# Performance work log

Measured on AMD Instinct MI355X. Metric: run time of the kernel, lower is better.

The kernel has to match this reference:

```python
import jax, jax.numpy as jnp
import numpy as np

B, C, H, W = 8, 128, 64, 64   # batch, hidden_dim, spatial
CIN = 192                      # input_dim
N, K, R, DFF = 1, 4, 8, 512    # d_state, scan dirs, dt_rank=ceil(128/16), mlp hidden
EPS = 1e-5


def _conv1x1(t, w, b=None):
    y = jnp.einsum('bchw,oc->bohw', t, w)
    return y + b[None, :, None, None] if b is not None else y


def _ln_cf(t, g, bta):
    # LayerNorm over channel dim (channel_first)
    mu = t.mean(1, keepdims=True)
    var = ((t - mu) ** 2).mean(1, keepdims=True)
    return (t - mu) * jax.lax.rsqrt(var + EPS) * g[None, :, None, None] + bta[None, :, None, None]


def _forward(h, cz, cr, cq, x,
             in_proj_w, in_proj_b, ln1_g, ln1_b,
             ssm_in_w, conv_w, conv_b,
             x_proj_w, dt_w, dt_b, A_logs, Ds,
             outnorm_g, outnorm_b, out_proj_w,
             ln2_g, ln2_b, fc1_w, fc1_b, fc2_w, fc2_b,
             gate_w, gate_b):
    combined = jnp.concatenate([h, x], axis=1)          # [B, C+CIN, H, W]
    feat = _conv1x1(combined, in_proj_w, in_proj_b)     # [B, C, H, W]

    # ---- SS2D (v2_noz, channel_first) ----
    u = _conv1x1(_ln_cf(feat, ln1_g, ln1_b), ssm_in_w)  # in_proj (no bias)
    u = jax.lax.conv_general_dilated(u, conv_w, (1, 1), [(1, 1), (1, 1)],
                                     dimension_numbers=('NCHW', 'OIHW', 'NCHW'),
                                     feature_group_count=C)
    u = jax.nn.silu(u + conv_b[None, :, None, None])

    L = H * W
    x0 = u.reshape(B, C, L)
    x1 = u.transpose(0, 1, 3, 2).reshape(B, C, L)       # column-major scan
    xs = jnp.stack([x0, x1, x0[..., ::-1], x1[..., ::-1]], axis=1)  # [B,K,C,L]

    x_dbl = jnp.einsum('bkcl,kdc->bkdl', xs, x_proj_w)  # [B,K,R+2N,L]
    dts, Bs, Cs = jnp.split(x_dbl, [R, R + N], axis=2)
    delta = jax.nn.softplus(jnp.einsum('bkrl,kcr->bkcl', dts, dt_w) + dt_b[None, :, :, None])
    A = -jnp.exp(A_logs).reshape(K, C, N)
    D = Ds.reshape(K, C)

    dA = jnp.exp(delta[..., None] * A[None, :, :, None, :])                   # [B,K,C,L,N]
    dBu = (delta * xs)[..., None] * Bs.transpose(0, 1, 3, 2)[:, :, None, :, :]  # [B,K,C,L,N]

    def step(hst, inp):
        dA_t, dBu_t, C_t = inp
        hst = dA_t * hst + dBu_t                         # [B,K,C,N]
        return hst, jnp.einsum('bkcn,bkn->bkc', hst, C_t)

    init = jnp.zeros((B, K, C, N), u.dtype)
    _, ys = jax.lax.scan(step, init,
                         (dA.transpose(3, 0, 1, 2, 4),
                          dBu.transpose(3, 0, 1, 2, 4),
                          Cs.transpose(3, 0, 1, 2)))
    ys = ys.transpose(1, 2, 3, 0)                        # [B,K,C,L]
    ys = ys + D[None, :, :, None] * xs

    # cross-merge: undo flips and transposes, sum directions
    y = ys[:, 0] + ys[:, 2, :, ::-1]
    y_t = ys[:, 1] + ys[:, 3, :, ::-1]
    y = y + y_t.reshape(B, C, W, H).transpose(0, 1, 3, 2).reshape(B, C, L)
    y = y.reshape(B, C, H, W)
    y = _ln_cf(y, outnorm_g, outnorm_b)
    ssm_out = _conv1x1(y, out_proj_w)

    # ---- VSSBlock residuals (drop_path identity in eval) ----
    z = feat + ssm_out
    m = _conv1x1(_ln_cf(z, ln2_g, ln2_b), fc1_w, fc1_b)
    m = jax.nn.gelu(m, approximate=False)
    m = _conv1x1(m, fc2_w, fc2_b)
    z = z + m

    # ---- gated update ----
    g = jax.nn.sigmoid(_conv1x1(z, gate_w, gate_b))
    return g * z + (1.0 - g) * h


def setup_inputs() -> dict:
    key = jax.random.key(0)
    ks = jax.random.split(key, 20)
    rn = lambda i, shape, s=0.02: jax.random.normal(ks[i], shape, jnp.float32) * s
    return dict(
        h=jax.random.normal(ks[0], (B, C, H, W), jnp.float32),
        cz=jax.random.normal(ks[1], (B, C, H, W), jnp.float32),
        cr=jax.random.normal(ks[2], (B, C, H, W), jnp.float32),
        cq=jax.random.normal(ks[3], (B, C, H, W), jnp.float32),
        x=jax.random.normal(ks[4], (B, CIN, H, W), jnp.float32),
        in_proj_w=rn(5, (C, C + CIN)), in_proj_b=jnp.zeros(C, jnp.float32),
        ln1_g=jnp.ones(C, jnp.float32), ln1_b=jnp.zeros(C, jnp.float32),
        ssm_in_w=rn(6, (C, C)),
        conv_w=rn(7, (C, 1, 3, 3), 0.1), conv_b=jnp.zeros(C, jnp.float32),
        x_proj_w=rn(8, (K, R + 2 * N, C)),
        dt_w=rn(9, (K, C, R), 0.1), dt_b=rn(10, (K, C), 0.1),
        A_logs=jnp.zeros((K * C, N), jnp.float32),
        Ds=jnp.ones(K * C, jnp.float32),
        outnorm_g=jnp.ones(C, jnp.float32), outnorm_b=jnp.zeros(C, jnp.float32),
        out_proj_w=rn(11, (C, C)),
        ln2_g=jnp.ones(C, jnp.float32), ln2_b=jnp.zeros(C, jnp.float32),
        fc1_w=rn(12, (DFF, C)), fc1_b=jnp.zeros(DFF, jnp.float32),
        fc2_w=rn(13, (C, DFF)), fc2_b=jnp.zeros(C, jnp.float32),
        gate_w=rn(14, (C, C)), gate_b=jnp.zeros(C, jnp.float32),
    )


def reference(h, cz, cr, cq, x,
              in_proj_w, in_proj_b, ln1_g, ln1_b,
              ssm_in_w, conv_w, conv_b,
              x_proj_w, dt_w, dt_b, A_logs, Ds,
              outnorm_g, outnorm_b, out_proj_w,
              ln2_g, ln2_b, fc1_w, fc1_b, fc2_w, fc2_b,
              gate_w, gate_b):
    return _forward(h, cz, cr, cq, x,
                    in_proj_w, in_proj_b, ln1_g, ln1_b,
                    ssm_in_w, conv_w, conv_b,
                    x_proj_w, dt_w, dt_b, A_logs, Ds,
                    outnorm_g, outnorm_b, out_proj_w,
                    ln2_g, ln2_b, fc1_w, fc1_b, fc2_w, fc2_b,
                    gate_w, gate_b)
```

## Files before the change

kernel.cpp:

```cpp
#include <hip/hip_runtime.h>
#include <hip/hip_bf16.h>

constexpr int B_ = 8, C_ = 128, Hh = 64, Ww = 64, L_ = Hh * Ww;
constexpr int CIN_ = 192, K_ = 4, Rr = 8, DFF_ = 512;
constexpr long SZ1 = (long)B_ * C_ * L_;
constexpr float EPSf = 1e-5f;
constexpr float LOG2E = 1.44269504088896f;
constexpr float LN2f  = 0.693147180559945f;

#define DEVI __device__ __forceinline__

using s16x4 = __attribute__((ext_vector_type(4))) short;
using s16x8 = __attribute__((ext_vector_type(8))) short;
using f32x4 = __attribute__((ext_vector_type(4))) float;

DEVI float sigm(float x) { return 1.f / (1.f + __expf(-x)); }
DEVI float geluf(float x) { return 0.5f * x * (1.f + erff(x * 0.70710678118654752f)); }
DEVI float siluf(float x) { return x * sigm(x); }

DEVI unsigned short f2bf(float f) {
    unsigned u = __float_as_uint(f);
    u += 0x7fffu + ((u >> 16) & 1u);
    return (unsigned short)(u >> 16);
}

DEVI int tadr(int pos) { return ((pos & 63) << 6) | (pos >> 6); }

template <int BN, bool ACC, bool BIAS, bool XGELU, bool SIG, bool GATE, bool SPLIT>
__global__ __launch_bounds__(256) void gemm_k(
    const float* __restrict__ W, const float* __restrict__ X1, long sX1,
    const float* __restrict__ X2, long sX2, int splitRow,
    const float* __restrict__ bias, float* __restrict__ Cp, long sC,
    int M, int N, int K)
{
    constexpr int NI = BN / 32;
    __shared__ unsigned short sA[128][40];
    __shared__ unsigned short sB[BN][40];
    const int tid = threadIdx.x;
    const int bn = blockIdx.x, bm = blockIdx.y, bz = blockIdx.z;
    const float* X1b = X1 + (long)bz * sX1;
    const float* X2b = (SPLIT || GATE) ? (X2 + (long)bz * sX2) : nullptr;
    float* Cb = Cp + (long)bz * sC;
    const int n0 = bn * BN, m0 = bm * 128;

    const int l = tid & 63, w = tid >> 6;
    const int wm = w >> 1, wn = w & 1;
    const int lr = l & 15, lk = (l >> 4) * 8;

    const int awrow = tid >> 1, awk = (tid & 1) * 16;

    f32x4 acc[4][NI];
#pragma unroll
    for (int i = 0; i < 4; i++)
#pragma unroll
        for (int j = 0; j < NI; j++) acc[i][j] = (f32x4)0.f;

    for (int k0 = 0; k0 < K; k0 += 32) {
        {
            const float* wp = W + (long)(m0 + awrow) * K + k0 + awk;
            float4 f0 = *(const float4*)(wp + 0);
            float4 f1 = *(const float4*)(wp + 4);
            float4 f2 = *(const float4*)(wp + 8);
            float4 f3 = *(const float4*)(wp + 12);
            s16x8 v0, v1;
            v0[0]=f2bf(f0.x); v0[1]=f2bf(f0.y); v0[2]=f2bf(f0.z); v0[3]=f2bf(f0.w);
            v0[4]=f2bf(f1.x); v0[5]=f2bf(f1.y); v0[6]=f2bf(f1.z); v0[7]=f2bf(f1.w);
            v1[0]=f2bf(f2.x); v1[1]=f2bf(f2.y); v1[2]=f2bf(f2.z); v1[3]=f2bf(f2.w);
            v1[4]=f2bf(f3.x); v1[5]=f2bf(f3.y); v1[6]=f2bf(f3.z); v1[7]=f2bf(f3.w);
            *(s16x8*)&sA[awrow][awk] = v0;
            *(s16x8*)&sA[awrow][awk + 8] = v1;
        }
        if constexpr (BN == 128) {
            const int bnb = tid & 31, bkb = tid >> 5;
            const int krow = k0 + bkb * 4;
            const float* xp;
            if (SPLIT && krow >= splitRow)
                xp = X2b + (long)(krow - splitRow) * N + n0 + bnb * 4;
            else
                xp = X1b + (long)krow * N + n0 + bnb * 4;
            float4 r0 = *(const float4*)(xp + 0 * (long)N);
            float4 r1 = *(const float4*)(xp + 1 * (long)N);
            float4 r2 = *(const float4*)(xp + 2 * (long)N);
            float4 r3 = *(const float4*)(xp + 3 * (long)N);
            if (XGELU) {
                r0.x=geluf(r0.x); r0.y=geluf(r0.y); r0.z=geluf(r0.z); r0.w=geluf(r0.w);
                r1.x=geluf(r1.x); r1.y=geluf(r1.y); r1.z=geluf(r1.z); r1.w=geluf(r1.w);
                r2.x=geluf(r2.x); r2.y=geluf(r2.y); r2.z=geluf(r2.z); r2.w=geluf(r2.w);
                r3.x=geluf(r3.x); r3.y=geluf(r3.y); r3.z=geluf(r3.z); r3.w=geluf(r3.w);
            }
            const float* p0 = (const float*)&r0;
            const float* p1 = (const float*)&r1;
            const float* p2 = (const float*)&r2;
            const float* p3 = (const float*)&r3;
#pragma unroll
            for (int c = 0; c < 4; c++) {
                s16x4 v;
                v[0] = f2bf(p0[c]); v[1] = f2bf(p1[c]);
                v[2] = f2bf(p2[c]); v[3] = f2bf(p3[c]);
                *(s16x4*)&sB[bnb * 4 + c][bkb * 4] = v;
            }
        } else {
            const int bnb = tid & 15, bkb = tid >> 4;
            const int krow = k0 + bkb * 2;
            const int col0 = n0 + bnb * 4;
            const float* xpa;
            const float* xpb;
            if (SPLIT && krow >= splitRow)
                xpa = X2b + (long)(krow - splitRow) * N + col0;
            else
                xpa = X1b + (long)krow * N + col0;
            if (SPLIT && (krow + 1) >= splitRow)
                xpb = X2b + (long)(krow + 1 - splitRow) * N + col0;
            else
                xpb = X1b + (long)(krow + 1) * N + col0;
            float4 r0 = *(const float4*)xpa;
            float4 r1 = *(const float4*)xpb;
            if (XGELU) {
                r0.x=geluf(r0.x); r0.y=geluf(r0.y); r0.z=geluf(r0.z); r0.w=geluf(r0.w);
                r1.x=geluf(r1.x); r1.y=geluf(r1.y); r1.z=geluf(r1.z); r1.w=geluf(r1.w);
            }
            const float* p0 = (const float*)&r0;
            const float* p1 = (const float*)&r1;
#pragma unroll
            for (int c = 0; c < 4; c++) {
                unsigned v = (unsigned)f2bf(p0[c]) | ((unsigned)f2bf(p1[c]) << 16);
                *(unsigned*)&sB[bnb * 4 + c][bkb * 2] = v;
            }
        }
        __syncthreads();
        s16x8 af[4], bf[NI];
#pragma unroll
        for (int mi = 0; mi < 4; mi++) af[mi] = *(const s16x8*)&sA[wm * 64 + mi * 16 + lr][lk];
#pragma unroll
        for (int ni = 0; ni < NI; ni++) bf[ni] = *(const s16x8*)&sB[wn * (BN / 2) + ni * 16 + lr][lk];
#pragma unroll
        for (int mi = 0; mi < 4; mi++)
#pragma unroll
            for (int ni = 0; ni < NI; ni++)
                acc[mi][ni] = __builtin_amdgcn_mfma_f32_16x16x32_bf16(af[mi], bf[ni], acc[mi][ni], 0, 0, 0);
        __syncthreads();
    }

#pragma unroll
    for (int mi = 0; mi < 4; mi++) {
#pragma unroll
        for (int r = 0; r < 4; r++) {
            const int row = m0 + wm * 64 + mi * 16 + (l >> 4) * 4 + r;
            const float bv = BIAS ? bias[row] : 0.f;
#pragma unroll
            for (int ni = 0; ni < NI; ni++) {
                const int col = n0 + wn * (BN / 2) + ni * 16 + lr;
                float* cp = Cb + (long)row * N + col;
                float v = acc[mi][ni][r] + bv;
                if (ACC) v += *cp;
                if (SIG) v = sigm(v);
                if (GATE) {
                    v = sigm(v);
                    float zv = X1b[(long)row * N + col];
                    float hv = X2b[(long)row * N + col];
                    v = hv + v * (zv - hv);
                }
                *cp = v;
            }
        }
    }
}

__global__ __launch_bounds__(256) void ln_cf_k(const float* __restrict__ in,
                                               const float* __restrict__ g,
                                               const float* __restrict__ bta,
                                               float* __restrict__ out)
{
    __shared__ float s1[4][64], s2[4][64];
    const int tid = threadIdx.x;
    const int p = tid & 63, q = tid >> 6;
    const long posg = (long)blockIdx.x * 64 + p;
    const int b = (int)(posg / L_);
    const int pp = (int)(posg % L_);
    const float* base = in + ((long)b * C_ + q * 32) * L_ + pp;
    float v[32];
    float s = 0.f, sq = 0.f;
#pragma unroll
    for (int i = 0; i < 32; i++) {
        float t = base[(long)i * L_];
        v[i] = t; s += t; sq += t * t;
    }
    s1[q][p] = s; s2[q][p] = sq;
    __syncthreads();
    float ts = s1[0][p] + s1[1][p] + s1[2][p] + s1[3][p];
    float tq = s2[0][p] + s2[1][p] + s2[2][p] + s2[3][p];
    float mu = ts * (1.f / 128.f);
    float var = tq * (1.f / 128.f) - mu * mu;
    float rs = rsqrtf(var + EPSf);
    float* ob = out + ((long)b * C_ + q * 32) * L_ + pp;
#pragma unroll
    for (int i = 0; i < 32; i++) {
        int c = q * 32 + i;
        ob[(long)i * L_] = (v[i] - mu) * rs * g[c] + bta[c];
    }
}

__global__ __launch_bounds__(256) void dwconvT_k(const float* __restrict__ in,
                                                 const float* __restrict__ wts,
                                                 const float* __restrict__ bias,
                                                 float* __restrict__ uo,
                                                 float* __restrict__ uTo)
{
    __shared__ float t[64][65];
    const long plane = blockIdx.x;
    const int c = (int)(plane & 127);
    const int tid = threadIdx.x;
    const float* src = in + plane * (long)L_;
#pragma unroll
    for (int ii = 0; ii < 16; ii++) {
        int idx = tid + ii * 256;
        t[idx >> 6][idx & 63] = src[idx];
    }
    float kw[9];
#pragma unroll
    for (int q = 0; q < 9; q++) kw[q] = wts[c * 9 + q];
    const float bc = bias[c];
    __syncthreads();
    float r[16];
#pragma unroll
    for (int ii = 0; ii < 16; ii++) {
        int idx = tid + ii * 256;
        int h = idx >> 6, w2 = idx & 63;
        float acc = bc;
#pragma unroll
        for (int dh = -1; dh <= 1; dh++) {
            int hh = h + dh;
            if ((unsigned)hh >= 64u) continue;
#pragma unroll
            for (int dw = -1; dw <= 1; dw++) {
                int ww2 = w2 + dw;
                if ((unsigned)ww2 >= 64u) continue;
                acc += t[hh][ww2] * kw[(dh + 1) * 3 + (dw + 1)];
            }
        }
        r[ii] = siluf(acc);
    }
    __syncthreads();
    float* ud = uo + plane * (long)L_;
#pragma unroll
    for (int ii = 0; ii < 16; ii++) {
        int idx = tid + ii * 256;
        t[idx >> 6][idx & 63] = r[ii];
        ud[idx] = r[ii];
    }
    __syncthreads();
    float* utd = uTo + plane * (long)L_;
#pragma unroll
    for (int ii = 0; ii < 16; ii++) {
        int idx = tid + ii * 256;
        utd[idx] = t[idx & 63][idx >> 6];
    }
}

template <bool ADD>
__global__ __launch_bounds__(256) void transp_k(const float* __restrict__ src,
                                                float* __restrict__ dst)
{
    __shared__ float t[64][65];
    const long plane = blockIdx.x;
    const float* s = src + plane * (long)L_;
    float* d = dst + plane * (long)L_;
    const int tid = threadIdx.x;
#pragma unroll
    for (int i = 0; i < 16; i++) {
        int idx = tid + i * 256;
        t[idx >> 6][idx & 63] = s[idx];
    }
    __syncthreads();
#pragma unroll
    for (int i = 0; i < 16; i++) {
        int idx = tid + i * 256;
        int r = idx >> 6, cc = idx & 63;
        float val = t[cc][r];
        if (ADD) d[idx] += val; else d[idx] = val;
    }
}

__global__ __launch_bounds__(256) void xdbl2_k(const float* __restrict__ u,
                                               const float* __restrict__ uT,
                                               const float* __restrict__ xw,
                                               float* __restrict__ out)
{
    __shared__ float wsm[2][16][132];
    const int pair = blockIdx.y, b = blockIdx.z;
    const int tid = threadIdx.x;
#pragma unroll
    for (int i = 0; i < 8; i++) {
        int idx = tid * 8 + i;
        wsm[0][idx >> 7][idx & 127] = xw[pair * 2048 + idx];
        wsm[1][idx >> 7][idx & 127] = xw[(pair + 2) * 2048 + idx];
    }
    __syncthreads();
    const int dg = (tid & 3) * 4;
    const int lo = tid >> 2;
    const int pos = blockIdx.x * 64 + lo;
    const float* usrc = (pair ? uT : u) + (long)b * C_ * L_ + pos;
    float a0[4] = {0.f, 0.f, 0.f, 0.f};
    float a1[4] = {0.f, 0.f, 0.f, 0.f};
#pragma unroll 4
    for (int c = 0; c < C_; c++) {
        float uc = usrc[(long)c * L_];
#pragma unroll
        for (int j = 0; j < 4; j++) {
            a0[j] += wsm[0][dg + j][c] * uc;
            a1[j] += wsm[1][dg + j][c] * uc;
        }
    }
    const long baseA = ((long)(b * K_ + pair) * L_) << 4;
    const long baseB = ((long)(b * K_ + pair + 2) * L_) << 4;
    const int s  = tadr(pos);
    const int s2 = tadr(L_ - 1 - pos);
    *(float4*)(out + baseA + ((long)s  << 4) + dg) = make_float4(a0[0], a0[1], a0[2], a0[3]);
    *(float4*)(out + baseB + ((long)s2 << 4) + dg) = make_float4(a1[0], a1[1], a1[2], a1[3]);
}

__global__ __launch_bounds__(256) void scan_ph1L_k(const float* __restrict__ xdbl,
                                                   const float* __restrict__ u,
                                                   const float* __restrict__ uT,
                                                   const float* __restrict__ dtw,
                                                   const float* __restrict__ dtb,
                                                   const float* __restrict__ alogs,
                                                   float* __restrict__ st)
{
    __shared__ float xtf[2][32][16];
    __shared__ float xtb[2][32][16];
    const int bid = blockIdx.x;
    const int jj = bid & 63, kh = (bid >> 6) & 1, b = bid >> 7;
    const int t = threadIdx.x;
    const int kf = kh, kb = kh + 2;
    const float* xf = xdbl + ((long)(b * 4 + kf) << 16);
    const float* xb = xdbl + ((long)(b * 4 + kb) << 16);
    {
        const int q = t & 3, i = (t >> 2) & 31, j2 = t >> 7;
        const int jf = 2 * jj + j2, jB = 127 - jf;
        const int sf = (((jf & 1) * 32 + i) << 6) | (jf >> 1);
        const int sb = (((jB & 1) * 32 + i) << 6) | (jB >> 1);
        *(float4*)&xtf[j2][i][q * 4] = *(const float4*)(xf + (long)sf * 16 + q * 4);
        *(float4*)&xtb[j2][i][q * 4] = *(const float4*)(xb + (long)sb * 16 + q * 4);
    }
    const int c = t & 127, jh = t >> 7;
    const int jf = 2 * jj + jh, jB = 127 - jf;
    const float* uplane = (kh ? uT : u) + (long)(b * 128 + c) * L_;
    float ur[32];
    {
        const float* up = uplane + jf * 32;
#pragma unroll
        for (int q = 0; q < 8; q++) *(float4*)&ur[q * 4] = *(const float4*)(up + q * 4);
    }
    __syncthreads();
    {
        float dw[8];
#pragma unroll
        for (int r = 0; r < 8; r++) dw[r] = dtw[((kf * 128 + c) << 3) + r];
        const float db = dtb[kf * 128 + c];
        float An[4];
#pragma unroll
        for (int n = 0; n < 4; n++) An[n] = -__expf(alogs[((kf * 128 + c) << 2) + n]);
        float P0 = 1.f, P1 = 1.f, P2 = 1.f, P3 = 1.f;
        float S0 = 0.f, S1 = 0.f, S2 = 0.f, S3 = 0.f;
#pragma unroll
        for (int i = 0; i < 32; i++) {
            const float* xr = xtf[jh][i];
            float z = db + xr[0]*dw[0] + xr[1]*dw[1] + xr[2]*dw[2] + xr[3]*dw[3]
                         + xr[4]*dw[4] + xr[5]*dw[5] + xr[6]*dw[6] + xr[7]*dw[7];
            float wv = (z > 15.f) ? z * LOG2E : log2f(1.f + __expf(z));
            float dl = wv * LN2f;
            float du = dl * ur[i];
            float e;
            e = exp2f(wv * An[0]); S0 = e * S0 + du * xr[8];  P0 *= e;
            e = exp2f(wv * An[1]); S1 = e * S1 + du * xr[9];  P1 *= e;
            e = exp2f(wv * An[2]); S2 = e * S2 + du * xr[10]; P2 *= e;
            e = exp2f(wv * An[3]); S3 = e * S3 + du * xr[11]; P3 *= e;
        }
        float* o = st + ((long)((b * 4 + kf) * 128 + c) << 10) + (jf << 3);
        *(float4*)o = make_float4(P0, P1, P2, P3);
        *(float4*)(o + 4) = make_float4(S0, S1, S2, S3);
    }
    {
        float dw[8];
#pragma unroll
        for (int r = 0; r < 8; r++) dw[r] = dtw[((kb * 128 + c) << 3) + r];
        const float db = dtb[kb * 128 + c];
        float An[4];
#pragma unroll
        for (int n = 0; n < 4; n++) An[n] = -__expf(alogs[((kb * 128 + c) << 2) + n]);
        float P0 = 1.f, P1 = 1.f, P2 = 1.f, P3 = 1.f;
        float S0 = 0.f, S1 = 0.f, S2 = 0.f, S3 = 0.f;
#pragma unroll
        for (int i = 0; i < 32; i++) {
            const float* xr = xtb[jh][i];
            float z = db + xr[0]*dw[0] + xr[1]*dw[1] + xr[2]*dw[2] + xr[3]*dw[3]
                         + xr[4]*dw[4] + xr[5]*dw[5] + xr[6]*dw[6] + xr[7]*dw[7];
            float wv = (z > 15.f) ? z * LOG2E : log2f(1.f + __expf(z));
            float dl = wv * LN2f;
            float du = dl * ur[31 - i];
            float e;
            e = exp2f(wv * An[0]); S0 = e * S0 + du * xr[8];  P0 *= e;
            e = exp2f(wv * An[1]); S1 = e * S1 + du * xr[9];  P1 *= e;
            e = exp2f(wv * An[2]); S2 = e * S2 + du * xr[10]; P2 *= e;
            e = exp2f(wv * An[3]); S3 = e * S3 + du * xr[11]; P3 *= e;
        }
        float* o = st + ((long)((b * 4 + kb) * 128 + c) << 10) + (jB << 3);
        *(float4*)o = make_float4(P0, P1, P2, P3);
        *(float4*)(o + 4) = make_float4(S0, S1, S2, S3);
    }
}

__global__ __launch_bounds__(256) void scan_mid_k(float* __restrict__ st)
{
    const long t = (long)blockIdx.x * 256 + threadIdx.x;
    const long chain = t >> 6;
    const int ln = (int)(t & 63);
    float* base = st + (chain << 10) + (ln << 4);
    float4 Pa = *(float4*)(base + 0);
    float4 Sa = *(float4*)(base + 4);
    float4 Pb = *(float4*)(base + 8);
    float4 Sb = *(float4*)(base + 12);
    float4 P, S;
    P.x = Pb.x * Pa.x; P.y = Pb.y * Pa.y; P.z = Pb.z * Pa.z; P.w = Pb.w * Pa.w;
    S.x = Sb.x + Pb.x * Sa.x; S.y = Sb.y + Pb.y * Sa.y;
    S.z = Sb.z + Pb.z * Sa.z; S.w = Sb.w + Pb.w * Sa.w;
#pragma unroll
    for (int d = 1; d < 64; d <<= 1) {
        float4 Pu, Su;
        Pu.x = __shfl_up(P.x, d, 64); Pu.y = __shfl_up(P.y, d, 64);
        Pu.z = __shfl_up(P.z, d, 64); Pu.w = __shfl_up(P.w, d, 64);
        Su.x = __shfl_up(S.x, d, 64); Su.y = __shfl_up(S.y, d, 64);
        Su.z = __shfl_up(S.z, d, 64); Su.w = __shfl_up(S.w, d, 64);
        if (ln >= d) {
            S.x += P.x * Su.x; S.y += P.y * Su.y;
            S.z += P.z * Su.z; S.w += P.w * Su.w;
            P.x *= Pu.x; P.y *= Pu.y; P.z *= Pu.z; P.w *= Pu.w;
        }
    }
    float4 E;
    E.x = __shfl_up(S.x, 1, 64); E.y = __shfl_up(S.y, 1, 64);
    E.z = __shfl_up(S.z, 1, 64); E.w = __shfl_up(S.w, 1, 64);
    if (ln == 0) { E.x = 0.f; E.y = 0.f; E.z = 0.f; E.w = 0.f; }
    float4 E1;
    E1.x = Sa.x + Pa.x * E.x; E1.y = Sa.y + Pa.y * E.y;
    E1.z = Sa.z + Pa.z * E.z; E1.w = Sa.w + Pa.w * E.w;
    *(float4*)(base + 4)  = E;
    *(float4*)(base + 12) = E1;
}

__global__ __launch_bounds__(256) void scan_ph2L_k(const float* __restrict__ xdbl,
                                                   const float* __restrict__ u,
                                                   const float* __restrict__ uT,
                                                   const float* __restrict__ dtw,
                                                   const float* __restrict__ dtb,
                                                   const float* __restrict__ alogs,
                                                   const float* __restrict__ Dsp,
                                                   const float* __restrict__ st,
                                                   float* __restrict__ Y0,
                                                   float* __restrict__ Yt)
{
    __shared__ float xtf[2][32][16];
    __shared__ float xtb[2][32][16];
    __shared__ float yt[128][65];
    const int bid = blockIdx.x;
    const int jj = bid & 63, kh = (bid >> 6) & 1, b = bid >> 7;
    const int t = threadIdx.x;
    const int kf = kh, kb = kh + 2;
    const float* xf = xdbl + ((long)(b * 4 + kf) << 16);
    const float* xb = xdbl + ((long)(b * 4 + kb) << 16);
    {
        const int q = t & 3, i = (t >> 2) & 31, j2 = t >> 7;
        const int jf = 2 * jj + j2, jB = 127 - jf;
        const int sf = (((jf & 1) * 32 + i) << 6) | (jf >> 1);
        const int sb = (((jB & 1) * 32 + i) << 6) | (jB >> 1);
        *(float4*)&xtf[j2][i][q * 4] = *(const float4*)(xf + (long)sf * 16 + q * 4);
        *(float4*)&xtb[j2][i][q * 4] = *(const float4*)(xb + (long)sb * 16 + q * 4);
    }
    const int c = t & 127, jh = t >> 7;
    const int jf = 2 * jj + jh, jB = 127 - jf;
    const float* uplane = (kh ? uT : u) + (long)(b * 128 + c) * L_;
    float ur[32];
    {
        const float* up = uplane + jf * 32;
#pragma unroll
        for (int q = 0; q < 8; q++) *(float4*)&ur[q * 4] = *(const float4*)(up + q * 4);
    }
    __syncthreads();
    {
        float dw[8];
#pragma unroll
        for (int r = 0; r < 8; r++) dw[r] = dtw[((kf * 128 + c) << 3) + r];
        const float db = dtb[kf * 128 + c];
        float An[4];
#pragma unroll
        for (int n = 0; n < 4; n++) An[n] = -__expf(alogs[((kf * 128 + c) << 2) + n]);
        const float Dc = Dsp[kf * 128 + c];
        float4 H = *(const float4*)(st + ((long)((b * 4 + kf) * 128 + c) << 10) + (jf << 3) + 4);
        float h0 = H.x, h1 = H.y, h2 = H.z, h3 = H.w;
#pragma unroll
        for (int i = 0; i < 32; i++) {
            const float* xr = xtf[jh][i];
            float z = db + xr[0]*dw[0] + xr[1]*dw[1] + xr[2]*dw[2] + xr[3]*dw[3]
                         + xr[4]*dw[4] + xr[5]*dw[5] + xr[6]*dw[6] + xr[7]*dw[7];
            float wv = (z > 15.f) ? z * LOG2E : log2f(1.f + __expf(z));
            float dl = wv * LN2f;
            float du = dl * ur[i];
            float e;
            e = exp2f(wv * An[0]); h0 = e * h0 + du * xr[8];
            e = exp2f(wv * An[1]); h1 = e * h1 + du * xr[9];
            e = exp2f(wv * An[2]); h2 = e * h2 + du * xr[10];
            e = exp2f(wv * An[3]); h3 = e * h3 + du * xr[11];
            yt[c][jh * 32 + i] = h0 * xr[12] + h1 * xr[13] + h2 * xr[14] + h3 * xr[15] + Dc * ur[i];
        }
    }
    {
        float dw[8];
#pragma unroll
        for (int r = 0; r < 8; r++) dw[r] = dtw[((kb * 128 + c) << 3) + r];
        const float db = dtb[kb * 128 + c];
        float An[4];
#pragma unroll
        for (int n = 0; n < 4; n++) An[n] = -__expf(alogs[((kb * 128 + c) << 2) + n]);
        const float Dc = Dsp[kb * 128 + c];
        float4 H = *(const float4*)(st + ((long)((b * 4 + kb) * 128 + c) << 10) + (jB << 3) + 4);
        float h0 = H.x, h1 = H.y, h2 = H.z, h3 = H.w;
#pragma unroll
        for (int i = 0; i < 32; i++) {
            const float* xr = xtb[jh][i];
            float z = db + xr[0]*dw[0] + xr[1]*dw[1] + xr[2]*dw[2] + xr[3]*dw[3]
                         + xr[4]*dw[4] + xr[5]*dw[5] + xr[6]*dw[6] + xr[7]*dw[7];
            float wv = (z > 15.f) ? z * LOG2E : log2f(1.f + __expf(z));
            float dl = wv * LN2f;
            float uv = ur[31 - i];
            float du = dl * uv;
            float e;
            e = exp2f(wv * An[0]); h0 = e * h0 + du * xr[8];
            e = exp2f(wv * An[1]); h1 = e * h1 + du * xr[9];
            e = exp2f(wv * An[2]); h2 = e * h2 + du * xr[10];
            e = exp2f(wv * An[3]); h3 = e * h3 + du * xr[11];
            yt[c][jh * 32 + 31 - i] += h0 * xr[12] + h1 * xr[13] + h2 * xr[14] + h3 * xr[15] + Dc * uv;
        }
    }
    __syncthreads();
    float* ydst = (kh ? Yt : Y0) + (long)(b * 128) * L_ + jj * 64;
    const int pos = t & 63, cg = t >> 6;
#pragma unroll
    for (int rep = 0; rep < 32; rep++) {
        const int c2 = cg + rep * 4;
        ydst[(long)c2 * L_ + pos] = yt[c2][pos];
    }
}

extern "C" void kernel_launch(void* const* d_in, const int* in_sizes, int n_in,
                              void* d_out, int out_size, void* d_ws, size_t ws_size,
                              hipStream_t stream)
{
    const float* h_in      = (const float*)d_in[0];
    const float* x_in      = (const float*)d_in[4];
    const float* in_proj_w = (const float*)d_in[5];
    const float* in_proj_b = (const float*)d_in[6];
    const float* ln1_g     = (const float*)d_in[7];
    const float* ln1_b     = (const float*)d_in[8];
    const float* ssm_in_w  = (const float*)d_in[9];
    const float* conv_w    = (const float*)d_in[10];
    const float* conv_b    = (const float*)d_in[11];
    const float* x_proj_w  = (const float*)d_in[12];
    const float* dt_w      = (const float*)d_in[13];
    const float* dt_b      = (const float*)d_in[14];
    const float* A_logs    = (const float*)d_in[15];
    const float* Dsp       = (const float*)d_in[16];
    const float* outnorm_g = (const float*)d_in[17];
    const float* outnorm_b = (const float*)d_in[18];
    const float* out_proj_w= (const float*)d_in[19];
    const float* ln2_g     = (const float*)d_in[20];
    const float* ln2_b     = (const float*)d_in[21];
    const float* fc1_w     = (const float*)d_in[22];
    const float* fc1_b     = (const float*)d_in[23];
    const float* fc2_w     = (const float*)d_in[24];
    const float* fc2_b     = (const float*)d_in[25];
    const float* gate_w    = (const float*)d_in[26];
    const float* gate_b    = (const float*)d_in[27];

    float* ws   = (float*)d_ws;
    float* fz   = ws;
    float* ubuf = ws + SZ1;
    float* tbuf = ws + 2 * SZ1;
    float* ybuf = ws + 3 * SZ1;
    float* xdbl = ws + 4 * SZ1;
    float* stbf = ws + 4 * SZ1 + 2097152;
    float* mbuf = ubuf;
    float* gbuf = (float*)d_out;

    const dim3 blk(256);
    const long sBC = (long)C_ * L_;
    const long sX  = (long)CIN_ * L_;
    const long sM  = (long)DFF_ * L_;

    gemm_k<64, false, true, false, false, false, true><<<dim3(64, 1, 8), blk, 0, stream>>>(
        in_proj_w, h_in, sBC, x_in, sX, 128, in_proj_b, fz, sBC, 128, L_, 320);
    ln_cf_k<<<dim3(512), blk, 0, stream>>>(fz, ln1_g, ln1_b, ybuf);
    gemm_k<64, false, false, false, false, false, false><<<dim3(64, 1, 8), blk, 0, stream>>>(
        ssm_in_w, ybuf, sBC, nullptr, 0, 1 << 30, nullptr, tbuf, sBC, 128, L_, 128);
    dwconvT_k<<<dim3(1024), blk, 0, stream>>>(tbuf, conv_w, conv_b, ubuf, ybuf);
    xdbl2_k<<<dim3(64, 2, 8), blk, 0, stream>>>(ubuf, ybuf, x_proj_w, xdbl);
    scan_ph1L_k<<<dim3(1024), blk, 0, stream>>>(xdbl, ubuf, ybuf, dt_w, dt_b, A_logs, stbf);
    scan_mid_k<<<dim3(1024), blk, 0, stream>>>(stbf);
    scan_ph2L_k<<<dim3(1024), blk, 0, stream>>>(xdbl, ubuf, ybuf, dt_w, dt_b,
                                                A_logs, Dsp, stbf, tbuf, gbuf);
    transp_k<true><<<dim3(1024), blk, 0, stream>>>(gbuf, tbuf);
    ln_cf_k<<<dim3(512), blk, 0, stream>>>(tbuf, outnorm_g, outnorm_b, ybuf);
    gemm_k<64, true, false, false, false, false, false><<<dim3(64, 1, 8), blk, 0, stream>>>(
        out_proj_w, ybuf, sBC, nullptr, 0, 1 << 30, nullptr, fz, sBC, 128, L_, 128);
    ln_cf_k<<<dim3(512), blk, 0, stream>>>(fz, ln2_g, ln2_b, gbuf);
    gemm_k<128, false, true, false, false, false, false><<<dim3(32, 4, 8), blk, 0, stream>>>(
        fc1_w, gbuf, sBC, nullptr, 0, 1 << 30, fc1_b, mbuf, sM, 512, L_, 128);
    gemm_k<64, true, true, true, false, false, false><<<dim3(64, 1, 8), blk, 0, stream>>>(
        fc2_w, mbuf, sM, nullptr, 0, 1 << 30, fc2_b, fz, sBC, 128, L_, 512);
    gemm_k<64, false, true, false, false, true, false><<<dim3(64, 1, 8), blk, 0, stream>>>(
        gate_w, fz, sBC, h_in, sBC, 1 << 30, gate_b, (float*)d_out, sBC, 128, L_, 128);
}
```

Baseline: 256.0 us.

## Fuse channel LayerNorms into GEMM prologue/epilogue and vectorize scan LDS reads

The first LayerNorm is folded into the in_proj GEMM epilogue, which reduces per-column statistics across the full 128-row M tile and writes the normalized output directly. For outnorm, a small stats-only kernel computes mean and rstd, and the out_proj GEMM applies the normalization while loading its B operand. That same GEMM then also emits the ln2 output in its epilogue. This removes three full read+write passes of the activation tensor and two kernel launches, at the cost of extra registers and shared memory in the GEMM. The scan loops also replace scalar shared-memory reads with float4 loads.

```diff
diff --git a/kernel.cpp b/kernel.cpp
--- a/kernel.cpp
+++ b/kernel.cpp
@@ -26,12 +26,16 @@
 
 DEVI int tadr(int pos) { return ((pos & 63) << 6) | (pos >> 6); }
 
-template <int BN, bool ACC, bool BIAS, bool XGELU, bool SIG, bool GATE, bool SPLIT>
+template <int BN, bool ACC, bool BIAS, bool XGELU, bool SIG, bool GATE, bool SPLIT,
+          bool XLN, bool LNOUT>
 __global__ __launch_bounds__(256) void gemm_k(
     const float* __restrict__ W, const float* __restrict__ X1, long sX1,
     const float* __restrict__ X2, long sX2, int splitRow,
-    const float* __restrict__ bias, float* __restrict__ Cp, long sC,
-    int M, int N, int K)
+    const float* __restrict__ bias,
+    const float* __restrict__ xmu, const float* __restrict__ xrs,
+    const float* __restrict__ xg, const float* __restrict__ xbt,
+    float* __restrict__ NOut, const float* __restrict__ og, const float* __restrict__ obt,
+    float* __restrict__ Cp, long sC, int M, int N, int K)
 {
     constexpr int NI = BN / 32;
     __shared__ unsigned short sA[128][40];
@@ -115,6 +119,16 @@
                 xpb = X1b + (long)(krow + 1) * N + col0;
             float4 r0 = *(const float4*)xpa;
             float4 r1 = *(const float4*)xpb;
+            if (XLN) {
+                float4 m4 = *(const float4*)(xmu + (long)bz * N + col0);
+                float4 s4 = *(const float4*)(xrs + (long)bz * N + col0);
+                float ga = xg[krow], be = xbt[krow];
+                r0.x=(r0.x-m4.x)*s4.x*ga+be; r0.y=(r0.y-m4.y)*s4.y*ga+be;
+                r0.z=(r0.z-m4.z)*s4.z*ga+be; r0.w=(r0.w-m4.w)*s4.w*ga+be;
+                ga = xg[krow + 1]; be = xbt[krow + 1];
+                r1.x=(r1.x-m4.x)*s4.x*ga+be; r1.y=(r1.y-m4.y)*s4.y*ga+be;
+                r1.z=(r1.z-m4.z)*s4.z*ga+be; r1.w=(r1.w-m4.w)*s4.w*ga+be;
+            }
             if (XGELU) {
                 r0.x=geluf(r0.x); r0.y=geluf(r0.y); r0.z=geluf(r0.z); r0.w=geluf(r0.w);
                 r1.x=geluf(r1.x); r1.y=geluf(r1.y); r1.z=geluf(r1.z); r1.w=geluf(r1.w);
@@ -141,6 +155,11 @@
         __syncthreads();
     }
 
+    float ps[NI], pq[NI];
+    if (LNOUT) {
+#pragma unroll
+        for (int ni = 0; ni < NI; ni++) { ps[ni] = 0.f; pq[ni] = 0.f; }
+    }
 #pragma unroll
     for (int mi = 0; mi < 4; mi++) {
 #pragma unroll
@@ -161,15 +180,66 @@
                     v = hv + v * (zv - hv);
                 }
                 *cp = v;
-            }
-        }
-    }
-}
-
-__global__ __launch_bounds__(256) void ln_cf_k(const float* __restrict__ in,
-                                               const float* __restrict__ g,
-                                               const float* __restrict__ bta,
-                                               float* __restrict__ out)
+                if (LNOUT) {
+                    acc[mi][ni][r] = v;
+                    ps[ni] += v; pq[ni] += v * v;
+                }
+            }
+        }
+    }
+    if constexpr (LNOUT) {
+        __shared__ float redS[2][2][NI][16];
+        __shared__ float redQ[2][2][NI][16];
+        __shared__ float muL[BN], rsL[BN];
+#pragma unroll
+        for (int ni = 0; ni < NI; ni++) {
+            ps[ni] += __shfl_xor(ps[ni], 16, 64);
+            ps[ni] += __shfl_xor(ps[ni], 32, 64);
+            pq[ni] += __shfl_xor(pq[ni], 16, 64);
+            pq[ni] += __shfl_xor(pq[ni], 32, 64);
+        }
+        if (l < 16) {
+#pragma unroll
+            for (int ni = 0; ni < NI; ni++) {
+                redS[wm][wn][ni][l] = ps[ni];
+                redQ[wm][wn][ni][l] = pq[ni];
+            }
+        }
+        __syncthreads();
+        if (tid < BN) {
+            const int cc = tid;
+            const int wn2 = cc >> 5, rem = cc & 31;
+            const int ni2 = rem >> 4, lr2 = rem & 15;
+            float s = redS[0][wn2][ni2][lr2] + redS[1][wn2][ni2][lr2];
+            float q = redQ[0][wn2][ni2][lr2] + redQ[1][wn2][ni2][lr2];
+            float mu = s * (1.f / 128.f);
+            float var = q * (1.f / 128.f) - mu * mu;
+            muL[cc] = mu;
+            rsL[cc] = rsqrtf(var + EPSf);
+        }
+        __syncthreads();
+        float* Nb = NOut + (long)bz * sC;
+#pragma unroll
+        for (int mi = 0; mi < 4; mi++) {
+#pragma unroll
+            for (int r = 0; r < 4; r++) {
+                const int row = m0 + wm * 64 + mi * 16 + (l >> 4) * 4 + r;
+                const float gg = og[row], bb = obt[row];
+#pragma unroll
+                for (int ni = 0; ni < NI; ni++) {
+                    const int cc = wn * (BN / 2) + ni * 16 + lr;
+                    const int col = n0 + cc;
+                    float v = acc[mi][ni][r];
+                    Nb[(long)row * N + col] = (v - muL[cc]) * rsL[cc] * gg + bb;
+                }
+            }
+        }
+    }
+}
+
+__global__ __launch_bounds__(256) void ln_stats_k(const float* __restrict__ in,
+                                                  float* __restrict__ mu,
+                                                  float* __restrict__ rs)
 {
     __shared__ float s1[4][64], s2[4][64];
     const int tid = threadIdx.x;
@@ -178,25 +248,21 @@
     const int b = (int)(posg / L_);
     const int pp = (int)(posg % L_);
     const float* base = in + ((long)b * C_ + q * 32) * L_ + pp;
-    float v[32];
     float s = 0.f, sq = 0.f;
 #pragma unroll
     for (int i = 0; i < 32; i++) {
         float t = base[(long)i * L_];
-        v[i] = t; s += t; sq += t * t;
+        s += t; sq += t * t;
     }
     s1[q][p] = s; s2[q][p] = sq;
     __syncthreads();
-    float ts = s1[0][p] + s1[1][p] + s1[2][p] + s1[3][p];
-    float tq = s2[0][p] + s2[1][p] + s2[2][p] + s2[3][p];
-    float mu = ts * (1.f / 128.f);
-    float var = tq * (1.f / 128.f) - mu * mu;
-    float rs = rsqrtf(var + EPSf);
-    float* ob = out + ((long)b * C_ + q * 32) * L_ + pp;
-#pragma unroll
-    for (int i = 0; i < 32; i++) {
-        int c = q * 32 + i;
-        ob[(long)i * L_] = (v[i] - mu) * rs * g[c] + bta[c];
+    if (q == 0) {
+        float ts = s1[0][p] + s1[1][p] + s1[2][p] + s1[3][p];
+        float tq = s2[0][p] + s2[1][p] + s2[2][p] + s2[3][p];
+        float m = ts * (1.f / 128.f);
+        float var = tq * (1.f / 128.f) - m * m;
+        mu[posg] = m;
+        rs[posg] = rsqrtf(var + EPSf);
     }
 }
 
@@ -365,17 +431,19 @@
         float S0 = 0.f, S1 = 0.f, S2 = 0.f, S3 = 0.f;
 #pragma unroll
         for (int i = 0; i < 32; i++) {
-            const float* xr = xtf[jh][i];
-            float z = db + xr[0]*dw[0] + xr[1]*dw[1] + xr[2]*dw[2] + xr[3]*dw[3]
-                         + xr[4]*dw[4] + xr[5]*dw[5] + xr[6]*dw[6] + xr[7]*dw[7];
+            float4 x0 = *(const float4*)&xtf[jh][i][0];
+            float4 x1 = *(const float4*)&xtf[jh][i][4];
+            float4 xs = *(const float4*)&xtf[jh][i][8];
+            float z = db + x0.x*dw[0] + x0.y*dw[1] + x0.z*dw[2] + x0.w*dw[3]
+                         + x1.x*dw[4] + x1.y*dw[5] + x1.z*dw[6] + x1.w*dw[7];
             float wv = (z > 15.f) ? z * LOG2E : log2f(1.f + __expf(z));
             float dl = wv * LN2f;
             float du = dl * ur[i];
             float e;
-            e = exp2f(wv * An[0]); S0 = e * S0 + du * xr[8];  P0 *= e;
-            e = exp2f(wv * An[1]); S1 = e * S1 + du * xr[9];  P1 *= e;
-            e = exp2f(wv * An[2]); S2 = e * S2 + du * xr[10]; P2 *= e;
-            e = exp2f(wv * An[3]); S3 = e * S3 + du * xr[11]; P3 *= e;
+            e = exp2f(wv * An[0]); S0 = e * S0 + du * xs.x; P0 *= e;
+            e = exp2f(wv * An[1]); S1 = e * S1 + du * xs.y; P1 *= e;
+            e = exp2f(wv * An[2]); S2 = e * S2 + du * xs.z; P2 *= e;
+            e = exp2f(wv * An[3]); S3 = e * S3 + du * xs.w; P3 *= e;
         }
         float* o = st + ((long)((b * 4 + kf) * 128 + c) << 10) + (jf << 3);
         *(float4*)o = make_float4(P0, P1, P2, P3);
@@ -393,17 +461,19 @@
         float S0 = 0.f, S1 = 0.f, S2 = 0.f, S3 = 0.f;
 #pragma unroll
         for (int i = 0; i < 32; i++) {
-            const float* xr = xtb[jh][i];
-            float z = db + xr[0]*dw[0] + xr[1]*dw[1] + xr[2]*dw[2] + xr[3]*dw[3]
-                         + xr[4]*dw[4] + xr[5]*dw[5] + xr[6]*dw[6] + xr[7]*dw[7];
+            float4 x0 = *(const float4*)&xtb[jh][i][0];
+            float4 x1 = *(const float4*)&xtb[jh][i][4];
+            float4 xs = *(const float4*)&xtb[jh][i][8];
+            float z = db + x0.x*dw[0] + x0.y*dw[1] + x0.z*dw[2] + x0.w*dw[3]
+                         + x1.x*dw[4] + x1.y*dw[5] + x1.z*dw[6] + x1.w*dw[7];
             float wv = (z > 15.f) ? z * LOG2E : log2f(1.f + __expf(z));
             float dl = wv * LN2f;
             float du = dl * ur[31 - i];
             float e;
-            e = exp2f(wv * An[0]); S0 = e * S0 + du * xr[8];  P0 *= e;
-            e = exp2f(wv * An[1]); S1 = e * S1 + du * xr[9];  P1 *= e;
-            e = exp2f(wv * An[2]); S2 = e * S2 + du * xr[10]; P2 *= e;
-            e = exp2f(wv * An[3]); S3 = e * S3 + du * xr[11]; P3 *= e;
+            e = exp2f(wv * An[0]); S0 = e * S0 + du * xs.x; P0 *= e;
+            e = exp2f(wv * An[1]); S1 = e * S1 + du * xs.y; P1 *= e;
+            e = exp2f(wv * An[2]); S2 = e * S2 + du * xs.z; P2 *= e;
+            e = exp2f(wv * An[3]); S3 = e * S3 + du * xs.w; P3 *= e;
         }
         float* o = st + ((long)((b * 4 + kb) * 128 + c) << 10) + (jB << 3);
         *(float4*)o = make_float4(P0, P1, P2, P3);
@@ -500,18 +570,21 @@
         float h0 = H.x, h1 = H.y, h2 = H.z, h3 = H.w;
 #pragma unroll
         for (int i = 0; i < 32; i++) {
-            const float* xr = xtf[jh][i];
-            float z = db + xr[0]*dw[0] + xr[1]*dw[1] + xr[2]*dw[2] + xr[3]*dw[3]
-                         + xr[4]*dw[4] + xr[5]*dw[5] + xr[6]*dw[6] + xr[7]*dw[7];
+            float4 x0 = *(const float4*)&xtf[jh][i][0];
+            float4 x1 = *(const float4*)&xtf[jh][i][4];
+            float4 xs = *(const float4*)&xtf[jh][i][8];
+            float4 xc = *(const float4*)&xtf[jh][i][12];
+            float z = db + x0.x*dw[0] + x0.y*dw[1] + x0.z*dw[2] + x0.w*dw[3]
+                         + x1.x*dw[4] + x1.y*dw[5] + x1.z*dw[6] + x1.w*dw[7];
             float wv = (z > 15.f) ? z * LOG2E : log2f(1.f + __expf(z));
             float dl = wv * LN2f;
             float du = dl * ur[i];
             float e;
-            e = exp2f(wv * An[0]); h0 = e * h0 + du * xr[8];
-            e = exp2f(wv * An[1]); h1 = e * h1 + du * xr[9];
-            e = exp2f(wv * An[2]); h2 = e * h2 + du * xr[10];
-            e = exp2f(wv * An[3]); h3 = e * h3 + du * xr[11];
-            yt[c][jh * 32 + i] = h0 * xr[12] + h1 * xr[13] + h2 * xr[14] + h3 * xr[15] + Dc * ur[i];
+            e = exp2f(wv * An[0]); h0 = e * h0 + du * xs.x;
+            e = exp2f(wv * An[1]); h1 = e * h1 + du * xs.y;
+            e = exp2f(wv * An[2]); h2 = e * h2 + du * xs.z;
+            e = exp2f(wv * An[3]); h3 = e * h3 + du * xs.w;
+            yt[c][jh * 32 + i] = h0 * xc.x + h1 * xc.y + h2 * xc.z + h3 * xc.w + Dc * ur[i];
         }
     }
     {
@@ -527,19 +600,22 @@
         float h0 = H.x, h1 = H.y, h2 = H.z, h3 = H.w;
 #pragma unroll
         for (int i = 0; i < 32; i++) {
-            const float* xr = xtb[jh][i];
-            float z = db + xr[0]*dw[0] + xr[1]*dw[1] + xr[2]*dw[2] + xr[3]*dw[3]
-                         + xr[4]*dw[4] + xr[5]*dw[5] + xr[6]*dw[6] + xr[7]*dw[7];
+            float4 x0 = *(const float4*)&xtb[jh][i][0];
+            float4 x1 = *(const float4*)&xtb[jh][i][4];
+            float4 xs = *(const float4*)&xtb[jh][i][8];
+            float4 xc = *(const float4*)&xtb[jh][i][12];
+            float z = db + x0.x*dw[0] + x0.y*dw[1] + x0.z*dw[2] + x0.w*dw[3]
+                         + x1.x*dw[4] + x1.y*dw[5] + x1.z*dw[6] + x1.w*dw[7];
             float wv = (z > 15.f) ? z * LOG2E : log2f(1.f + __expf(z));
             float dl = wv * LN2f;
             float uv = ur[31 - i];
             float du = dl * uv;
             float e;
-            e = exp2f(wv * An[0]); h0 = e * h0 + du * xr[8];
-            e = exp2f(wv * An[1]); h1 = e * h1 + du * xr[9];
-            e = exp2f(wv * An[2]); h2 = e * h2 + du * xr[10];
-            e = exp2f(wv * An[3]); h3 = e * h3 + du * xr[11];
-            yt[c][jh * 32 + 31 - i] += h0 * xr[12] + h1 * xr[13] + h2 * xr[14] + h3 * xr[15] + Dc * uv;
+            e = exp2f(wv * An[0]); h0 = e * h0 + du * xs.x;
+            e = exp2f(wv * An[1]); h1 = e * h1 + du * xs.y;
+            e = exp2f(wv * An[2]); h2 = e * h2 + du * xs.z;
+            e = exp2f(wv * An[3]); h3 = e * h3 + du * xs.w;
+            yt[c][jh * 32 + 31 - i] += h0 * xc.x + h1 * xc.y + h2 * xc.z + h3 * xc.w + Dc * uv;
         }
     }
     __syncthreads();
@@ -589,6 +665,8 @@
     float* ybuf = ws + 3 * SZ1;
     float* xdbl = ws + 4 * SZ1;
     float* stbf = ws + 4 * SZ1 + 2097152;
+    float* muB  = stbf;
+    float* rsB  = stbf + 32768;
     float* mbuf = ubuf;
     float* gbuf = (float*)d_out;
 
@@ -597,11 +675,16 @@
     const long sX  = (long)CIN_ * L_;
     const long sM  = (long)DFF_ * L_;
 
-    gemm_k<64, false, true, false, false, false, true><<<dim3(64, 1, 8), blk, 0, stream>>>(
-        in_proj_w, h_in, sBC, x_in, sX, 128, in_proj_b, fz, sBC, 128, L_, 320);
-    ln_cf_k<<<dim3(512), blk, 0, stream>>>(fz, ln1_g, ln1_b, ybuf);
-    gemm_k<64, false, false, false, false, false, false><<<dim3(64, 1, 8), blk, 0, stream>>>(
-        ssm_in_w, ybuf, sBC, nullptr, 0, 1 << 30, nullptr, tbuf, sBC, 128, L_, 128);
+    gemm_k<64, false, true, false, false, false, true, false, true>
+        <<<dim3(64, 1, 8), blk, 0, stream>>>(
+        in_proj_w, h_in, sBC, x_in, sX, 128, in_proj_b,
+        nullptr, nullptr, nullptr, nullptr, ybuf, ln1_g, ln1_b,
+        fz, sBC, 128, L_, 320);
+    gemm_k<64, false, false, false, false, false, false, false, false>
+        <<<dim3(64, 1, 8), blk, 0, stream>>>(
+        ssm_in_w, ybuf, sBC, nullptr, 0, 1 << 30, nullptr,
+        nullptr, nullptr, nullptr, nullptr, nullptr, nullptr, nullptr,
+        tbuf, sBC, 128, L_, 128);
     dwconvT_k<<<dim3(1024), blk, 0, stream>>>(tbuf, conv_w, conv_b, ubuf, ybuf);
     xdbl2_k<<<dim3(64, 2, 8), blk, 0, stream>>>(ubuf, ybuf, x_proj_w, xdbl);
     scan_ph1L_k<<<dim3(1024), blk, 0, stream>>>(xdbl, ubuf, ybuf, dt_w, dt_b, A_logs, stbf);
@@ -609,14 +692,25 @@
     scan_ph2L_k<<<dim3(1024), blk, 0, stream>>>(xdbl, ubuf, ybuf, dt_w, dt_b,
                                                 A_logs, Dsp, stbf, tbuf, gbuf);
     transp_k<true><<<dim3(1024), blk, 0, stream>>>(gbuf, tbuf);
-    ln_cf_k<<<dim3(512), blk, 0, stream>>>(tbuf, outnorm_g, outnorm_b, ybuf);
-    gemm_k<64, true, false, false, false, false, false><<<dim3(64, 1, 8), blk, 0, stream>>>(
-        out_proj_w, ybuf, sBC, nullptr, 0, 1 << 30, nullptr, fz, sBC, 128, L_, 128);
-    ln_cf_k<<<dim3(512), blk, 0, stream>>>(fz, ln2_g, ln2_b, gbuf);
-    gemm_k<128, false, true, false, false, false, false><<<dim3(32, 4, 8), blk, 0, stream>>>(
-        fc1_w, gbuf, sBC, nullptr, 0, 1 << 30, fc1_b, mbuf, sM, 512, L_, 128);
-    gemm_k<64, true, true, true, false, false, false><<<dim3(64, 1, 8), blk, 0, stream>>>(
-        fc2_w, mbuf, sM, nullptr, 0, 1 << 30, fc2_b, fz, sBC, 128, L_, 512);
-    gemm_k<64, false, true, false, false, true, false><<<dim3(64, 1, 8), blk, 0, stream>>>(
-        gate_w, fz, sBC, h_in, sBC, 1 << 30, gate_b, (float*)d_out, sBC, 128, L_, 128);
-}
+    ln_stats_k<<<dim3(512), blk, 0, stream>>>(tbuf, muB, rsB);
+    gemm_k<64, true, false, false, false, false, false, true, true>
+        <<<dim3(64, 1, 8), blk, 0, stream>>>(
+        out_proj_w, tbuf, sBC, nullptr, 0, 1 << 30, nullptr,
+        muB, rsB, outnorm_g, outnorm_b, gbuf, ln2_g, ln2_b,
+        fz, sBC, 128, L_, 128);
+    gemm_k<128, false, true, false, false, false, false, false, false>
+        <<<dim3(32, 4, 8), blk, 0, stream>>>(
+        fc1_w, gbuf, sBC, nullptr, 0, 1 << 30, fc1_b,
+        nullptr, nullptr, nullptr, nullptr, nullptr, nullptr, nullptr,
+        mbuf, sM, 512, L_, 128);
+    gemm_k<64, true, true, true, false, false, false, false, false>
+        <<<dim3(64, 1, 8), blk, 0, stream>>>(
+        fc2_w, mbuf, sM, nullptr, 0, 1 << 30, fc2_b,
+        nullptr, nullptr, nullptr, nullptr, nullptr, nullptr, nullptr,
+        fz, sBC, 128, L_, 512);
+    gemm_k<64, false, true, false, false, true, false, false, false>
+        <<<dim3(64, 1, 8), blk, 0, stream>>>(
+        gate_w, fz, sBC, h_in, sBC, 1 << 30, gate_b,
+        nullptr, nullptr, nullptr, nullptr, nullptr, nullptr, nullptr,
+        (float*)d_out, sBC, 128, L_, 128);
+}
```

New measurement: 244.7 us. -4.4%, faster.
